# Kernel optimization log

Hardware: AMD Instinct MI355X
Metric: run time of the kernel (lower is better)

Reference implementation:

```python
import jax, jax.numpy as jnp
import numpy as np

N_NODES = 100000
N_EDGES = 1250000
IN_F = 128
OUT_F = 64


def setup_inputs() -> dict:
    key = jax.random.key(0)
    k1, k2, k3, k4 = jax.random.split(key, 4)
    x = jax.random.normal(k1, (N_NODES, IN_F), dtype=jnp.float32)
    weight = jax.random.normal(k2, (IN_F, OUT_F), dtype=jnp.float32) * (6.0 / (IN_F + OUT_F)) ** 0.5
    bias = jnp.zeros((OUT_F,), dtype=jnp.float32)
    edge_weight = jax.random.uniform(k3, (N_EDGES,), dtype=jnp.float32)
    edge_index = jax.random.randint(k4, (2, N_EDGES), 0, N_NODES, dtype=jnp.int64)
    return {"x": x, "weight": weight, "bias": bias, "edge_weight": edge_weight, "edge_index": edge_index}


def reference(x, weight, bias, edge_weight, edge_index):
    # Linear transform: [N, in] @ [in, out] -> [N, out]
    h = x @ weight
    src, dst = edge_index[0], edge_index[1]
    # Gather source node features, scale by edge weight: [E, out]
    x_j = h[src] * edge_weight[:, None]
    n = x.shape[0]
    # scatter_add of messages and edge counts per destination node
    out = jax.ops.segment_sum(x_j, dst, num_segments=n)
    count = jax.ops.segment_sum(jnp.ones_like(edge_weight), dst, num_segments=n)
    out = out / jnp.clip(count, 1.0)[:, None]  # scatter_mean with min-count 1
    out = out + bias
    return jax.nn.relu(out)
```

## Files before the change

kernel.cpp:

```cpp
#include <hip/hip_runtime.h>

#define N_NODES 100000
#define N_EDGES 1250000
#define IN_F 128
#define OUT_F 64

#define TM 64
__global__ __launch_bounds__(256) void gemm3_k(const float* __restrict__ x,
                                               const float* __restrict__ w,
                                               float* __restrict__ h) {
    __shared__ float wlds[IN_F * OUT_F];
    __shared__ float xlds[TM * IN_F];
    const int t = threadIdx.x;
    const int row0 = blockIdx.x * TM;

    const float4* w4p = (const float4*)w;
    float4* wl4 = (float4*)wlds;
    #pragma unroll
    for (int i = 0; i < 8; ++i) wl4[t + i * 256] = w4p[t + i * 256];

    #pragma unroll
    for (int i = 0; i < 8; ++i) {
        const int idx = t + i * 256;
        const int r   = idx >> 5;
        const int k4  = idx & 31;
        float4 v = make_float4(0.f, 0.f, 0.f, 0.f);
        if (row0 + r < N_NODES)
            v = ((const float4*)(x + (size_t)(row0 + r) * IN_F))[k4];
        const int k4s = (k4 + r) & 31;
        *(float4*)&xlds[r * IN_F + k4s * 4] = v;
    }
    __syncthreads();

    const int colg = t & 15;
    const int rowg = t >> 4;
    float acc[4][4];
    #pragma unroll
    for (int i = 0; i < 4; ++i)
        #pragma unroll
        for (int j = 0; j < 4; ++j) acc[i][j] = 0.f;

    #pragma unroll 8
    for (int k4 = 0; k4 < 32; ++k4) {
        float4 wv[4];
        #pragma unroll
        for (int kk = 0; kk < 4; ++kk)
            wv[kk] = *(const float4*)&wlds[(k4 * 4 + kk) * OUT_F + colg * 4];
        #pragma unroll
        for (int i = 0; i < 4; ++i) {
            const int r = rowg * 4 + i;
            const int k4s = (k4 + r) & 31;
            const float4 xv = *(const float4*)&xlds[r * IN_F + k4s * 4];
            acc[i][0] += xv.x * wv[0].x + xv.y * wv[1].x + xv.z * wv[2].x + xv.w * wv[3].x;
            acc[i][1] += xv.x * wv[0].y + xv.y * wv[1].y + xv.z * wv[2].y + xv.w * wv[3].y;
            acc[i][2] += xv.x * wv[0].z + xv.y * wv[1].z + xv.z * wv[2].z + xv.w * wv[3].z;
            acc[i][3] += xv.x * wv[0].w + xv.y * wv[1].w + xv.z * wv[2].w + xv.w * wv[3].w;
        }
    }

    #pragma unroll
    for (int i = 0; i < 4; ++i) {
        const int r = row0 + rowg * 4 + i;
        if (r < N_NODES) {
            float4 v = make_float4(acc[i][0], acc[i][1], acc[i][2], acc[i][3]);
            *(float4*)&h[(size_t)r * OUT_F + colg * 4] = v;
        }
    }
}

__global__ __launch_bounds__(256) void hist_k(const int* __restrict__ dst,
                                              int* __restrict__ cnt) {
    const int e = blockIdx.x * 256 + threadIdx.x;
    if (e >= N_EDGES) return;
    atomicAdd(&cnt[dst[e]], 1);
}

#define SCAN_B 1024
__global__ __launch_bounds__(256) void scan1_k(const int* __restrict__ cnt,
                                               int* __restrict__ start,
                                               int* __restrict__ bsum) {
    __shared__ int lds[256];
    const int t = threadIdx.x;
    const int base = blockIdx.x * SCAN_B + t * 4;
    int v0 = 0, v1 = 0, v2 = 0, v3 = 0;
    if (base + 0 < N_NODES) v0 = cnt[base + 0];
    if (base + 1 < N_NODES) v1 = cnt[base + 1];
    if (base + 2 < N_NODES) v2 = cnt[base + 2];
    if (base + 3 < N_NODES) v3 = cnt[base + 3];
    const int s = v0 + v1 + v2 + v3;
    lds[t] = s;
    __syncthreads();
    #pragma unroll
    for (int off = 1; off < 256; off <<= 1) {
        const int add = (t >= off) ? lds[t - off] : 0;
        __syncthreads();
        lds[t] += add;
        __syncthreads();
    }
    const int excl = lds[t] - s;
    if (base + 0 < N_NODES) start[base + 0] = excl;
    if (base + 1 < N_NODES) start[base + 1] = excl + v0;
    if (base + 2 < N_NODES) start[base + 2] = excl + v0 + v1;
    if (base + 3 < N_NODES) start[base + 3] = excl + v0 + v1 + v2;
    if (t == 255) bsum[blockIdx.x] = lds[t];
}

#define NSCAN_BLOCKS ((N_NODES + SCAN_B - 1) / SCAN_B)
__global__ __launch_bounds__(128) void scan2_k(int* __restrict__ bsum) {
    __shared__ int lds[128];
    const int t = threadIdx.x;
    const int v = (t < NSCAN_BLOCKS) ? bsum[t] : 0;
    lds[t] = v;
    __syncthreads();
    #pragma unroll
    for (int off = 1; off < 128; off <<= 1) {
        const int add = (t >= off) ? lds[t - off] : 0;
        __syncthreads();
        lds[t] += add;
        __syncthreads();
    }
    if (t < NSCAN_BLOCKS) bsum[t] = lds[t] - v;
}

__global__ __launch_bounds__(256) void scan3_k(int* __restrict__ start,
                                               int* __restrict__ pos,
                                               const int* __restrict__ bsum) {
    const int i = blockIdx.x * 256 + threadIdx.x;
    if (i >= N_NODES) return;
    const int v = start[i] + bsum[i / SCAN_B];
    start[i] = v;
    pos[i] = v;
}

__global__ __launch_bounds__(256) void bucket_k(const int* __restrict__ src,
                                                const int* __restrict__ dst,
                                                const float* __restrict__ ew,
                                                int* __restrict__ pos,
                                                uint2* __restrict__ pairs) {
    const int e = blockIdx.x * 256 + threadIdx.x;
    if (e >= N_EDGES) return;
    const int d = dst[e];
    const int p = atomicAdd(&pos[d], 1);
    pairs[p] = make_uint2((unsigned)src[e], __float_as_uint(ew[e]));
}

__global__ __launch_bounds__(256) void accum_k(const float* __restrict__ h,
                                               const uint2* __restrict__ pairs,
                                               const int* __restrict__ start,
                                               const int* __restrict__ cnt,
                                               const float* __restrict__ bias,
                                               float* __restrict__ out) {
    const int node = blockIdx.x * 4 + (threadIdx.x >> 6);
    const int lane = threadIdx.x & 63;
    const int q  = lane >> 4;
    const int ql = lane & 15;
    const int s0 = start[node];
    const int c  = cnt[node];

    float4 acc = make_float4(0.f, 0.f, 0.f, 0.f);
    for (int i = s0 + q; i < s0 + c; i += 4) {
        const uint2 pr = pairs[i];
        const float wgt = __uint_as_float(pr.y);
        const float4 hv = ((const float4*)(h + (size_t)pr.x * OUT_F))[ql];
        acc.x += hv.x * wgt;
        acc.y += hv.y * wgt;
        acc.z += hv.z * wgt;
        acc.w += hv.w * wgt;
    }

    #pragma unroll
    for (int m = 16; m <= 32; m <<= 1) {
        acc.x += __shfl_xor(acc.x, m, 64);
        acc.y += __shfl_xor(acc.y, m, 64);
        acc.z += __shfl_xor(acc.z, m, 64);
        acc.w += __shfl_xor(acc.w, m, 64);
    }

    if (q == 0) {
        float cf = (float)c;
        if (cf < 1.f) cf = 1.f;
        const float inv = 1.0f / cf;
        const float4 b = ((const float4*)bias)[ql];
        float4 v;
        v.x = acc.x * inv + b.x;
        v.y = acc.y * inv + b.y;
        v.z = acc.z * inv + b.z;
        v.w = acc.w * inv + b.w;
        v.x = v.x > 0.f ? v.x : 0.f;
        v.y = v.y > 0.f ? v.y : 0.f;
        v.z = v.z > 0.f ? v.z : 0.f;
        v.w = v.w > 0.f ? v.w : 0.f;
        ((float4*)(out + (size_t)node * OUT_F))[ql] = v;
    }
}

__global__ __launch_bounds__(256) void scatter_k(const float* __restrict__ h,
                                                 const float* __restrict__ ew,
                                                 const int* __restrict__ src,
                                                 const int* __restrict__ dst,
                                                 float* __restrict__ out,
                                                 float* __restrict__ cnt) {
    const int e = blockIdx.x * 4 + (threadIdx.x >> 6);
    if (e >= N_EDGES) return;
    const int lane = threadIdx.x & 63;
    const int   s = src[e];
    const int   d = dst[e];
    const float w = ew[e];
    const float v = h[(long)s * OUT_F + lane] * w;
    atomicAdd(&out[(long)d * OUT_F + lane], v);
    if (lane == 0) atomicAdd(&cnt[d], 1.0f);
}

__global__ __launch_bounds__(256) void final_k(float* __restrict__ out,
                                               const float* __restrict__ cnt,
                                               const float* __restrict__ bias) {
    const int tid = blockIdx.x * 256 + threadIdx.x;
    if (tid >= N_NODES * OUT_F) return;
    const int n = tid >> 6;
    const int f = tid & 63;
    float c = cnt[n];
    if (c < 1.0f) c = 1.0f;
    float v = out[tid] / c + bias[f];
    out[tid] = v > 0.0f ? v : 0.0f;
}

extern "C" void kernel_launch(void* const* d_in, const int* in_sizes, int n_in,
                              void* d_out, int out_size, void* d_ws, size_t ws_size,
                              hipStream_t stream) {
    const float* x    = (const float*)d_in[0];
    const float* w    = (const float*)d_in[1];
    const float* bias = (const float*)d_in[2];
    const float* ew   = (const float*)d_in[3];
    const int*   ei   = (const int*)d_in[4];

    float* out = (float*)d_out;
    const int* src = ei;
    const int* dst = ei + N_EDGES;

    char* ws = (char*)d_ws;
    float* h     = (float*)(ws);
    int*   cnt   = (int*)(ws + 25600000);
    int*   start = (int*)(ws + 26000000);
    int*   pos   = (int*)(ws + 26400000);
    int*   bsum  = (int*)(ws + 26800000);
    uint2* pairs = (uint2*)(ws + 26801024);
    const size_t WS_NEEDED = 26801024 + (size_t)N_EDGES * sizeof(uint2);

    gemm3_k<<<(N_NODES + TM - 1) / TM, 256, 0, stream>>>(x, w, h);

    if (ws_size >= WS_NEEDED) {
        hipMemsetAsync(cnt, 0, N_NODES * sizeof(int), stream);
        hist_k<<<(N_EDGES + 255) / 256, 256, 0, stream>>>(dst, cnt);
        scan1_k<<<NSCAN_BLOCKS, 256, 0, stream>>>(cnt, start, bsum);
        scan2_k<<<1, 128, 0, stream>>>(bsum);
        scan3_k<<<(N_NODES + 255) / 256, 256, 0, stream>>>(start, pos, bsum);
        bucket_k<<<(N_EDGES + 255) / 256, 256, 0, stream>>>(src, dst, ew, pos, pairs);
        accum_k<<<N_NODES / 4, 256, 0, stream>>>(h, pairs, start, cnt, bias, out);
    } else {
        float* fcnt = (float*)cnt;
        hipMemsetAsync(out, 0, (size_t)N_NODES * OUT_F * sizeof(float), stream);
        hipMemsetAsync(fcnt, 0, N_NODES * sizeof(float), stream);
        scatter_k<<<(N_EDGES + 3) / 4, 256, 0, stream>>>(h, ew, src, dst, out, fcnt);
        final_k<<<(N_NODES * OUT_F + 255) / 256, 256, 0, stream>>>(out, fcnt, bias);
    }
}
```

Baseline: 327.9 us.

## Split CSR bucketing into eight virtual partitions to reduce atomic contention

Result: slower. 344.2 us (+5.0%).

```diff
diff --git a/kernel.cpp b/kernel.cpp
--- a/kernel.cpp
+++ b/kernel.cpp
@@ -68,25 +68,29 @@
     }
 }
 
-__global__ __launch_bounds__(256) void hist_k(const int* __restrict__ dst,
-                                              int* __restrict__ cnt) {
+#define NVID 8
+#define M8 (NVID * N_NODES)
+
+__global__ __launch_bounds__(256) void hist8_k(const int* __restrict__ dst,
+                                               int* __restrict__ cnt8) {
     const int e = blockIdx.x * 256 + threadIdx.x;
     if (e >= N_EDGES) return;
-    atomicAdd(&cnt[dst[e]], 1);
-}
-
-#define SCAN_B 1024
-__global__ __launch_bounds__(256) void scan1_k(const int* __restrict__ cnt,
-                                               int* __restrict__ start,
-                                               int* __restrict__ bsum) {
+    const int vid = (e >> 8) & (NVID - 1);
+    atomicAdd(&cnt8[vid * N_NODES + dst[e]], 1);
+}
+
+__global__ __launch_bounds__(256) void scan1g_k(const int* __restrict__ in,
+                                                int* __restrict__ out,
+                                                int* __restrict__ bsum,
+                                                const int M) {
     __shared__ int lds[256];
     const int t = threadIdx.x;
-    const int base = blockIdx.x * SCAN_B + t * 4;
+    const int base = blockIdx.x * 1024 + t * 4;
     int v0 = 0, v1 = 0, v2 = 0, v3 = 0;
-    if (base + 0 < N_NODES) v0 = cnt[base + 0];
-    if (base + 1 < N_NODES) v1 = cnt[base + 1];
-    if (base + 2 < N_NODES) v2 = cnt[base + 2];
-    if (base + 3 < N_NODES) v3 = cnt[base + 3];
+    if (base + 0 < M) v0 = in[base + 0];
+    if (base + 1 < M) v1 = in[base + 1];
+    if (base + 2 < M) v2 = in[base + 2];
+    if (base + 3 < M) v3 = in[base + 3];
     const int s = v0 + v1 + v2 + v3;
     lds[t] = s;
     __syncthreads();
@@ -98,74 +102,89 @@
         __syncthreads();
     }
     const int excl = lds[t] - s;
-    if (base + 0 < N_NODES) start[base + 0] = excl;
-    if (base + 1 < N_NODES) start[base + 1] = excl + v0;
-    if (base + 2 < N_NODES) start[base + 2] = excl + v0 + v1;
-    if (base + 3 < N_NODES) start[base + 3] = excl + v0 + v1 + v2;
+    if (base + 0 < M) out[base + 0] = excl;
+    if (base + 1 < M) out[base + 1] = excl + v0;
+    if (base + 2 < M) out[base + 2] = excl + v0 + v1;
+    if (base + 3 < M) out[base + 3] = excl + v0 + v1 + v2;
     if (t == 255) bsum[blockIdx.x] = lds[t];
 }
 
-#define NSCAN_BLOCKS ((N_NODES + SCAN_B - 1) / SCAN_B)
-__global__ __launch_bounds__(128) void scan2_k(int* __restrict__ bsum) {
-    __shared__ int lds[128];
+__global__ __launch_bounds__(256) void scan2g_k(int* __restrict__ bsum,
+                                                const int m) {
+    __shared__ int lds[256];
     const int t = threadIdx.x;
-    const int v = (t < NSCAN_BLOCKS) ? bsum[t] : 0;
-    lds[t] = v;
+    const int base = t * 4;
+    int v0 = 0, v1 = 0, v2 = 0, v3 = 0;
+    if (base + 0 < m) v0 = bsum[base + 0];
+    if (base + 1 < m) v1 = bsum[base + 1];
+    if (base + 2 < m) v2 = bsum[base + 2];
+    if (base + 3 < m) v3 = bsum[base + 3];
+    const int s = v0 + v1 + v2 + v3;
+    lds[t] = s;
     __syncthreads();
     #pragma unroll
-    for (int off = 1; off < 128; off <<= 1) {
+    for (int off = 1; off < 256; off <<= 1) {
         const int add = (t >= off) ? lds[t - off] : 0;
         __syncthreads();
         lds[t] += add;
         __syncthreads();
     }
-    if (t < NSCAN_BLOCKS) bsum[t] = lds[t] - v;
-}
-
-__global__ __launch_bounds__(256) void scan3_k(int* __restrict__ start,
-                                               int* __restrict__ pos,
-                                               const int* __restrict__ bsum) {
+    const int excl = lds[t] - s;
+    if (base + 0 < m) bsum[base + 0] = excl;
+    if (base + 1 < m) bsum[base + 1] = excl + v0;
+    if (base + 2 < m) bsum[base + 2] = excl + v0 + v1;
+    if (base + 3 < m) bsum[base + 3] = excl + v0 + v1 + v2;
+}
+
+__global__ __launch_bounds__(256) void scan3g_k(int* __restrict__ pos8,
+                                                const int* __restrict__ bsum,
+                                                const int M) {
     const int i = blockIdx.x * 256 + threadIdx.x;
-    if (i >= N_NODES) return;
-    const int v = start[i] + bsum[i / SCAN_B];
-    start[i] = v;
-    pos[i] = v;
-}
-
-__global__ __launch_bounds__(256) void bucket_k(const int* __restrict__ src,
-                                                const int* __restrict__ dst,
-                                                const float* __restrict__ ew,
-                                                int* __restrict__ pos,
-                                                uint2* __restrict__ pairs) {
+    if (i >= M) return;
+    pos8[i] += bsum[i >> 10];
+}
+
+__global__ __launch_bounds__(256) void bucket8_k(const int* __restrict__ src,
+                                                 const int* __restrict__ dst,
+                                                 const float* __restrict__ ew,
+                                                 int* __restrict__ pos8,
+                                                 uint2* __restrict__ pairs) {
     const int e = blockIdx.x * 256 + threadIdx.x;
     if (e >= N_EDGES) return;
+    const int vid = (e >> 8) & (NVID - 1);
     const int d = dst[e];
-    const int p = atomicAdd(&pos[d], 1);
+    const int p = atomicAdd(&pos8[vid * N_NODES + d], 1);
     pairs[p] = make_uint2((unsigned)src[e], __float_as_uint(ew[e]));
 }
 
-__global__ __launch_bounds__(256) void accum_k(const float* __restrict__ h,
-                                               const uint2* __restrict__ pairs,
-                                               const int* __restrict__ start,
-                                               const int* __restrict__ cnt,
-                                               const float* __restrict__ bias,
-                                               float* __restrict__ out) {
+__global__ __launch_bounds__(256) void accum8_k(const float* __restrict__ h,
+                                                const uint2* __restrict__ pairs,
+                                                const int* __restrict__ pos8,
+                                                const int* __restrict__ cnt8,
+                                                const float* __restrict__ bias,
+                                                float* __restrict__ out) {
     const int node = blockIdx.x * 4 + (threadIdx.x >> 6);
     const int lane = threadIdx.x & 63;
     const int q  = lane >> 4;
     const int ql = lane & 15;
-    const int s0 = start[node];
-    const int c  = cnt[node];
 
     float4 acc = make_float4(0.f, 0.f, 0.f, 0.f);
-    for (int i = s0 + q; i < s0 + c; i += 4) {
-        const uint2 pr = pairs[i];
-        const float wgt = __uint_as_float(pr.y);
-        const float4 hv = ((const float4*)(h + (size_t)pr.x * OUT_F))[ql];
-        acc.x += hv.x * wgt;
-        acc.y += hv.y * wgt;
-        acc.z += hv.z * wgt;
-        acc.w += hv.w * wgt;
+    int c_me = 0;
+    #pragma unroll
+    for (int vv = 0; vv < 2; ++vv) {
+        const int idx = (2 * q + vv) * N_NODES + node;
+        const int e1 = pos8[idx];
+        const int c8 = cnt8[idx];
+        c_me += c8;
+        for (int i = e1 - c8; i < e1; ++i) {
+            const uint2 pr = pairs[i];
+            const float wgt = __uint_as_float(pr.y);
+            const float4 hv = ((const float4*)(h + (size_t)pr.x * OUT_F))[ql];
+            acc.x += hv.x * wgt;
+            acc.y += hv.y * wgt;
+            acc.z += hv.z * wgt;
+            acc.w += hv.w * wgt;
+        }
     }
 
     #pragma unroll
@@ -175,9 +194,11 @@
         acc.z += __shfl_xor(acc.z, m, 64);
         acc.w += __shfl_xor(acc.w, m, 64);
     }
+    c_me += __shfl_xor(c_me, 16, 64);
+    c_me += __shfl_xor(c_me, 32, 64);
 
     if (q == 0) {
-        float cf = (float)c;
+        float cf = (float)c_me;
         if (cf < 1.f) cf = 1.f;
         const float inv = 1.0f / cf;
         const float4 b = ((const float4*)bias)[ql];
@@ -239,25 +260,25 @@
 
     char* ws = (char*)d_ws;
     float* h     = (float*)(ws);
-    int*   cnt   = (int*)(ws + 25600000);
-    int*   start = (int*)(ws + 26000000);
-    int*   pos   = (int*)(ws + 26400000);
-    int*   bsum  = (int*)(ws + 26800000);
-    uint2* pairs = (uint2*)(ws + 26801024);
-    const size_t WS_NEEDED = 26801024 + (size_t)N_EDGES * sizeof(uint2);
+    int*   cnt8  = (int*)(ws + 25600000);
+    int*   pos8  = (int*)(ws + 28800000);
+    int*   bsum  = (int*)(ws + 32000000);
+    uint2* pairs = (uint2*)(ws + 32004096);
+    const size_t WS_NEEDED = 32004096 + (size_t)N_EDGES * sizeof(uint2);
 
     gemm3_k<<<(N_NODES + TM - 1) / TM, 256, 0, stream>>>(x, w, h);
 
     if (ws_size >= WS_NEEDED) {
-        hipMemsetAsync(cnt, 0, N_NODES * sizeof(int), stream);
-        hist_k<<<(N_EDGES + 255) / 256, 256, 0, stream>>>(dst, cnt);
-        scan1_k<<<NSCAN_BLOCKS, 256, 0, stream>>>(cnt, start, bsum);
-        scan2_k<<<1, 128, 0, stream>>>(bsum);
-        scan3_k<<<(N_NODES + 255) / 256, 256, 0, stream>>>(start, pos, bsum);
-        bucket_k<<<(N_EDGES + 255) / 256, 256, 0, stream>>>(src, dst, ew, pos, pairs);
-        accum_k<<<N_NODES / 4, 256, 0, stream>>>(h, pairs, start, cnt, bias, out);
+        hipMemsetAsync(cnt8, 0, M8 * sizeof(int), stream);
+        hist8_k<<<(N_EDGES + 255) / 256, 256, 0, stream>>>(dst, cnt8);
+        const int nsb = (M8 + 1023) / 1024;
+        scan1g_k<<<nsb, 256, 0, stream>>>(cnt8, pos8, bsum, M8);
+        scan2g_k<<<1, 256, 0, stream>>>(bsum, nsb);
+        scan3g_k<<<(M8 + 255) / 256, 256, 0, stream>>>(pos8, bsum, M8);
+        bucket8_k<<<(N_EDGES + 255) / 256, 256, 0, stream>>>(src, dst, ew, pos8, pairs);
+        accum8_k<<<N_NODES / 4, 256, 0, stream>>>(h, pairs, pos8, cnt8, bias, out);
     } else {
-        float* fcnt = (float*)cnt;
+        float* fcnt = (float*)(ws + 25600000);
         hipMemsetAsync(out, 0, (size_t)N_NODES * OUT_F * sizeof(float), stream);
         hipMemsetAsync(fcnt, 0, N_NODES * sizeof(float), stream);
         scatter_k<<<(N_EDGES + 3) / 4, 256, 0, stream>>>(h, ew, src, dst, out, fcnt);
```
